# Optimization experiments

Hardware: AMD Instinct MI355X
Metric: run time of the kernel (lower is better)

Reference implementation:

```python
import jax, jax.numpy as jnp
import numpy as np

N_NODES = 50000
N_EDGES = 600000
NUM_RELS = 5
IN_CH = 768
HID = 128
OUT_CH = 128
REL_DIM = 200


def _segment_softmax(scores, seg, n):
    # numerically stable softmax over variable-size segments (destination nodes)
    m = jax.ops.segment_max(scores, seg, num_segments=n)
    e = jnp.exp(scores - m[seg])
    s = jax.ops.segment_sum(e, seg, num_segments=n)
    return e / s[seg]


def _hgn_conv(x, edge_index, edge_type, W, Wr, a, Wres, rel_tab, final):
    # x: [N, h_in]; W: [h, h_in]; Wr: [h, rel_dim]; a: [3h]; rel_tab: [R, rel_dim]
    src = edge_index[0]
    dst = edge_index[1]
    n = x.shape[0]
    h = W.shape[0]
    Wx = x @ W.T                      # [N, h] (shared by x_i, x_j, messages)
    rel = rel_tab[edge_type] @ Wr.T   # [E, h]
    aA, aB, aC = a[:h], a[h:2 * h], a[2 * h:]
    # a([Wx_i | Wx_j | Wr rel]) decomposed to avoid materializing the concat
    score = Wx[dst] @ aA + Wx[src] @ aB + rel @ aC   # [E]
    alpha = jax.nn.leaky_relu(score, 0.2)
    alpha = _segment_softmax(alpha, dst, n)
    agg = jax.ops.segment_sum(Wx[src] * alpha[:, None], dst, num_segments=n)
    out = jax.nn.elu(agg + x @ Wres.T)
    if final:
        out = out / jnp.maximum(jnp.linalg.norm(out, axis=1, keepdims=True), 1e-12)
    return out, alpha


def setup_inputs() -> dict:
    key = jax.random.key(0)
    ks = jax.random.split(key, 20)
    s = 0.02
    return {
        "x": jax.random.normal(ks[0], (N_NODES, IN_CH), jnp.float32),
        "edge_index": jax.random.randint(ks[1], (2, N_EDGES), 0, N_NODES, jnp.int64 if jax.config.jax_enable_x64 else jnp.int32),
        "edge_type": jax.random.randint(ks[2], (N_EDGES,), 0, NUM_RELS, jnp.int64 if jax.config.jax_enable_x64 else jnp.int32),
        "l1_W": jax.random.normal(ks[3], (HID, IN_CH), jnp.float32) * s,
        "l1_b": jnp.zeros((HID,), jnp.float32),
        "l2_W": jax.random.normal(ks[4], (OUT_CH, HID), jnp.float32) * s,
        "l2_b": jnp.zeros((OUT_CH,), jnp.float32),
        "W1": jax.random.normal(ks[5], (HID, HID), jnp.float32) * s,
        "Wr1": jax.random.normal(ks[6], (HID, REL_DIM), jnp.float32) * s,
        "a1": jax.random.normal(ks[7], (3 * HID,), jnp.float32) * s,
        "Wres1": jax.random.normal(ks[8], (HID, HID), jnp.float32) * s,
        "rel1": jax.random.normal(ks[9], (NUM_RELS, REL_DIM), jnp.float32),
        "W2": jax.random.normal(ks[10], (HID, HID), jnp.float32) * s,
        "Wr2": jax.random.normal(ks[11], (HID, REL_DIM), jnp.float32) * s,
        "a2": jax.random.normal(ks[12], (3 * HID,), jnp.float32) * s,
        "Wres2": jax.random.normal(ks[13], (HID, HID), jnp.float32) * s,
        "rel2": jax.random.normal(ks[14], (NUM_RELS, REL_DIM), jnp.float32),
    }


def reference(x, edge_index, edge_type, l1_W, l1_b, l2_W, l2_b,
              W1, Wr1, a1, Wres1, rel1, W2, Wr2, a2, Wres2, rel2):
    out = jax.nn.leaky_relu(x @ l1_W.T + l1_b, 0.01)
    # layer 1 (dropout is identity in eval mode)
    out, alpha = _hgn_conv(out, edge_index, edge_type, W1, Wr1, a1, Wres1, rel1, final=False)
    # layer 2: original code blends alpha into self.alpha but weights messages
    # with its own (unblended) softmax alpha, so pre_alpha does not affect output
    out, _ = _hgn_conv(out, edge_index, edge_type, W2, Wr2, a2, Wres2, rel2, final=True)
    out = jax.nn.leaky_relu(out @ l2_W.T + l2_b, 0.01)
    return out
```

## Files before the change

kernel.cpp:

```cpp
#include <hip/hip_runtime.h>

namespace {

typedef unsigned short ushort_t;
typedef unsigned int uint_t;
typedef __attribute__((ext_vector_type(8))) short bf16x8;
typedef __attribute__((ext_vector_type(4))) float f32x4;

constexpr int N   = 50000;
constexpr int E   = 600000;
constexpr int NR  = 5;
constexpr int KIN = 768;
constexpr int H   = 128;
constexpr int RD  = 200;

__device__ inline ushort_t f2b(float f){
  uint_t u = __builtin_bit_cast(uint_t, f);
  uint_t r = (u + 0x7FFFu + ((u >> 16) & 1u)) >> 16;
  return (ushort_t)r;
}
__device__ inline float b2f_lo(uint_t u){ return __builtin_bit_cast(float, u << 16); }
__device__ inline float b2f_hi(uint_t u){ return __builtin_bit_cast(float, u & 0xFFFF0000u); }
__device__ inline float b2f_us(ushort_t h){ return __builtin_bit_cast(float, ((uint_t)h) << 16); }
__device__ inline uint_t cvtpk(float lo, float hi){
  uint_t r;
  asm("v_cvt_pk_bf16_f32 %0, %1, %2" : "=v"(r) : "v"(lo), "v"(hi));
  return r;
}

__global__ void prep_k(const float* __restrict__ l1W, const float* __restrict__ W1,
                       const float* __restrict__ R1, const float* __restrict__ W2,
                       const float* __restrict__ R2, const float* __restrict__ l2W,
                       ushort_t* __restrict__ wts, int* __restrict__ deg,
                       const int* __restrict__ edst,
                       const float* __restrict__ rel1, const float* __restrict__ Wr1,
                       const float* __restrict__ a1, float* __restrict__ sC1,
                       const float* __restrict__ rel2, const float* __restrict__ Wr2,
                       const float* __restrict__ a2, float* __restrict__ sC2){
  constexpr int S0 = H * KIN;
  constexpr int S1 = H * H;
  int b = blockIdx.x, tid = threadIdx.x;
  if (b < 704){
    int i = b * 256 + tid;
    float v;
    if (i < S0) v = l1W[i];
    else {
      int j = i - S0, seg = j >> 14, off = j & (S1 - 1);
      const float* srcs[5] = {W1, R1, W2, R2, l2W};
      v = srcs[seg][off];
    }
    wts[i] = f2b(v);
  } else if (b < 706){
    int L = b - 704;
    const float* rel = L ? rel2 : rel1;
    const float* Wr  = L ? Wr2  : Wr1;
    const float* a   = L ? a2   : a1;
    float*       sC  = L ? sC2  : sC1;
    __shared__ float red[256];
    int n = tid >> 1, half = tid & 1;
    float aC = a[256 + n];
    for (int r = 0; r < NR; ++r){
      float p = 0.f;
      for (int k = half * 100; k < half * 100 + 100; ++k)
        p += rel[r * RD + k] * Wr[n * RD + k];
      red[tid] = p * aC;
      __syncthreads();
      for (int s = 128; s > 0; s >>= 1){
        if (tid < s) red[tid] += red[tid + s];
        __syncthreads();
      }
      if (tid == 0) sC[r] = red[0];
      __syncthreads();
    }
  } else {
    int e = (b - 706) * 256 + tid;
    if (e < E) atomicAdd(&deg[edst[e]], 1);
  }
}

__global__ void scan1_k(const int* __restrict__ deg, int* __restrict__ chunk,
                        int* __restrict__ bsums, int n){
  __shared__ int s[256];
  int tid = threadIdx.x, i = blockIdx.x * 256 + tid;
  int v = (i < n) ? deg[i] : 0;
  s[tid] = v; __syncthreads();
  for (int off = 1; off < 256; off <<= 1){
    int t = (tid >= off) ? s[tid - off] : 0;
    __syncthreads();
    s[tid] += t;
    __syncthreads();
  }
  if (i < n) chunk[i] = s[tid] - v;
  if (tid == 255) bsums[blockIdx.x] = s[255];
}

__global__ void scan2_k(const int* __restrict__ bsums, int* __restrict__ boffs, int nb){
  __shared__ int s[256];
  int tid = threadIdx.x;
  int v = (tid < nb) ? bsums[tid] : 0;
  s[tid] = v; __syncthreads();
  for (int off = 1; off < 256; off <<= 1){
    int t = (tid >= off) ? s[tid - off] : 0;
    __syncthreads();
    s[tid] += t;
    __syncthreads();
  }
  if (tid < nb) boffs[tid] = s[tid] - v;
}

__global__ void scan3_k(int* __restrict__ rowptr, const int* __restrict__ boffs,
                        int* __restrict__ cursor, int n, int total){
  int i = blockIdx.x * 256 + threadIdx.x;
  if (i < n){
    int v = rowptr[i] + boffs[blockIdx.x];
    rowptr[i] = v; cursor[i] = v;
  }
  if (i == 0) rowptr[n] = total;
}

__global__ void fill_k(const int* __restrict__ src, const int* __restrict__ dst,
                       const int* __restrict__ et, int* __restrict__ cursor,
                       int* __restrict__ cpk){
  int e = blockIdx.x * 256 + threadIdx.x;
  if (e < E){
    int d = dst[e];
    int p = atomicAdd(&cursor[d], 1);
    cpk[p] = src[e] | (et[e] << 16);
  }
}

template<int K1, int M1, bool AFP32, bool NORM, bool STORE1, int M2>
__device__ __forceinline__ void gfused_impl(
    const void* __restrict__ Ap, const ushort_t* __restrict__ Wb1,
    const float* __restrict__ bias1,
    const ushort_t* __restrict__ WxG, const int* __restrict__ rowptr,
    const int* __restrict__ cpk, const float* __restrict__ sAi,
    const float* __restrict__ sBi, const float* __restrict__ sCi,
    ushort_t* __restrict__ out1,
    const ushort_t* __restrict__ Wb2, const float* __restrict__ vec2,
    void* __restrict__ out2, float* __restrict__ sAo, float* __restrict__ sBo, int M)
{
  constexpr int BK = 64;
  constexpr int NT = K1 / BK;
  constexpr int SP = 72;
  constexpr int CP = 136;
  __shared__ __align__(16) ushort_t U[128 * CP];
  __shared__ __align__(16) ushort_t Cs[64 * CP];
  ushort_t* const As  = U;
  ushort_t* const Bs  = U + 64 * SP;
  ushort_t* const B2s = U;
  const int tid  = threadIdx.x;
  const int wave = tid >> 6, lane = tid & 63;
  const int l15  = lane & 15, quad = lane >> 4;
  const int row0 = blockIdx.x * 64;

  if (M1 == 2){
    const int grp = tid >> 4;
    const int l   = tid & 15;
    const int gb  = tid & 48;
    #pragma unroll 1
    for (int nb = 0; nb < 4; ++nb){
      int lrow = nb * 16 + grp;
      int node = row0 + lrow;
      uint4 o = make_uint4(0, 0, 0, 0);
      if (node < M){
        int p0 = rowptr[node], p1 = rowptr[node + 1];
        int dg = p1 - p0;
        float sa = sAi[node];
        float m = -1e30f, ssum = 0.f;
        float a[8];
        #pragma unroll
        for (int j = 0; j < 8; ++j) a[j] = 0.f;
        for (int c0 = 0; c0 < dg; c0 += 16){
          int cnt = dg - c0; if (cnt > 16) cnt = 16;
          bool ok = l < cnt;
          int pk = cpk[p0 + c0 + (ok ? l : 0)];
          float s = sa + sBi[pk & 0xFFFF] + sCi[pk >> 16];
          s = s > 0.f ? s : 0.2f * s;
          float sv = ok ? s : -1e30f;
          #pragma unroll
          for (int off = 8; off > 0; off >>= 1) sv = fmaxf(sv, __shfl_xor(sv, off, 16));
          float mn = fmaxf(m, sv);
          float corr = __expf(m - mn);
          ssum *= corr;
          #pragma unroll
          for (int j = 0; j < 8; ++j) a[j] *= corr;
          float ev = ok ? __expf(s - mn) : 0.f;
          float es = ev;
          #pragma unroll
          for (int off = 8; off > 0; off >>= 1) es += __shfl_xor(es, off, 16);
          ssum += es;
          m = mn;
          int png = ok ? pk : 0;
          for (int e = 0; e < cnt; e += 4){
            int b0l = gb + e;
            int pe0 = __shfl(png, b0l,     64), pe1 = __shfl(png, b0l + 1, 64);
            int pe2 = __shfl(png, b0l + 2, 64), pe3 = __shfl(png, b0l + 3, 64);
            float e0 = __shfl(ev, b0l,     64), e1 = __shfl(ev, b0l + 1, 64);
            float e2 = __shfl(ev, b0l + 2, 64), e3 = __shfl(ev, b0l + 3, 64);
            uint4 u0 = *reinterpret_cast<const uint4*>(WxG + (size_t)(pe0 & 0xFFFF) * 128 + l * 8);
            uint4 u1 = *reinterpret_cast<const uint4*>(WxG + (size_t)(pe1 & 0xFFFF) * 128 + l * 8);
            uint4 u2 = *reinterpret_cast<const uint4*>(WxG + (size_t)(pe2 & 0xFFFF) * 128 + l * 8);
            uint4 u3 = *reinterpret_cast<const uint4*>(WxG + (size_t)(pe3 & 0xFFFF) * 128 + l * 8);
            a[0] += e0 * b2f_lo(u0.x); a[1] += e0 * b2f_hi(u0.x);
            a[2] += e0 * b2f_lo(u0.y); a[3] += e0 * b2f_hi(u0.y);
            a[4] += e0 * b2f_lo(u0.z); a[5] += e0 * b2f_hi(u0.z);
            a[6] += e0 * b2f_lo(u0.w); a[7] += e0 * b2f_hi(u0.w);
            a[0] += e1 * b2f_lo(u1.x); a[1] += e1 * b2f_hi(u1.x);
            a[2] += e1 * b2f_lo(u1.y); a[3] += e1 * b2f_hi(u1.y);
            a[4] += e1 * b2f_lo(u1.z); a[5] += e1 * b2f_hi(u1.z);
            a[6] += e1 * b2f_lo(u1.w); a[7] += e1 * b2f_hi(u1.w);
            a[0] += e2 * b2f_lo(u2.x); a[1] += e2 * b2f_hi(u2.x);
            a[2] += e2 * b2f_lo(u2.y); a[3] += e2 * b2f_hi(u2.y);
            a[4] += e2 * b2f_lo(u2.z); a[5] += e2 * b2f_hi(u2.z);
            a[6] += e2 * b2f_lo(u2.w); a[7] += e2 * b2f_hi(u2.w);
            a[0] += e3 * b2f_lo(u3.x); a[1] += e3 * b2f_hi(u3.x);
            a[2] += e3 * b2f_lo(u3.y); a[3] += e3 * b2f_hi(u3.y);
            a[4] += e3 * b2f_lo(u3.z); a[5] += e3 * b2f_hi(u3.z);
            a[6] += e3 * b2f_lo(u3.w); a[7] += e3 * b2f_hi(u3.w);
          }
        }
        float inv = (dg > 0) ? 1.f / ssum : 0.f;
        o.x = cvtpk(a[0] * inv, a[1] * inv);
        o.y = cvtpk(a[2] * inv, a[3] * inv);
        o.z = cvtpk(a[4] * inv, a[5] * inv);
        o.w = cvtpk(a[6] * inv, a[7] * inv);
      }
      *reinterpret_cast<uint4*>(&Cs[lrow * CP + l * 8]) = o;
    }
  }

  f32x4 acc[8];
  #pragma unroll
  for (int t = 0; t < 8; ++t) acc[t] = (f32x4){0.f, 0.f, 0.f, 0.f};

  const int ar = tid >> 2, aq = tid & 3;
  const int agrow = row0 + ar;
  const bool aok = agrow < M;
  const int awoff = ar * SP + aq * 16;
  const int bn = tid >> 1, bs = (tid & 1) * 32;
  const ushort_t* bsrc = Wb1 + (size_t)bn * K1 + bs;

  float4 pf0, pf1, pf2, pf3;
  uint4  pu0, pu1;
  uint4  pb0, pb1, pb2, pb3;
  pf0 = pf1 = pf2 = pf3 = make_float4(0.f, 0.f, 0.f, 0.f);
  pu0 = pu1 = make_uint4(0, 0, 0, 0);

#define ISSUE_A(kk) do{ if (aok){                                               \
    if constexpr (AFP32){                                                       \
      const float* ap_ = (const float*)Ap + (size_t)agrow * K1 + (kk) + aq * 16; \
      pf0 = *reinterpret_cast<const float4*>(ap_);                              \
      pf1 = *reinterpret_cast<const float4*>(ap_ + 4);                          \
      pf2 = *reinterpret_cast<const float4*>(ap_ + 8);                          \
      pf3 = *reinterpret_cast<const float4*>(ap_ + 12);                         \
    } else {                                                                    \
      const ushort_t* apb_ = (const ushort_t*)Ap + (size_t)agrow * K1 + (kk) + aq * 16; \
      pu0 = *reinterpret_cast<const uint4*>(apb_);                              \
      pu1 = *reinterpret_cast<const uint4*>(apb_ + 8);                          \
    } } }while(0)

#define ISSUE_B(kk) do{                                                         \
    pb0 = *reinterpret_cast<const uint4*>(bsrc + (kk));                         \
    pb1 = *reinterpret_cast<const uint4*>(bsrc + (kk) + 8);                     \
    pb2 = *reinterpret_cast<const uint4*>(bsrc + (kk) + 16);                    \
    pb3 = *reinterpret_cast<const uint4*>(bsrc + (kk) + 24);                    \
  }while(0)

#define WRITE_AB() do{                                                          \
    uint4 av0_, av1_;                                                           \
    if constexpr (AFP32){                                                       \
      av0_.x = cvtpk(pf0.x, pf0.y); av0_.y = cvtpk(pf0.z, pf0.w);               \
      av0_.z = cvtpk(pf1.x, pf1.y); av0_.w = cvtpk(pf1.z, pf1.w);               \
      av1_.x = cvtpk(pf2.x, pf2.y); av1_.y = cvtpk(pf2.z, pf2.w);               \
      av1_.z = cvtpk(pf3.x, pf3.y); av1_.w = cvtpk(pf3.z, pf3.w);               \
    } else { av0_ = pu0; av1_ = pu1; }                                          \
    *reinterpret_cast<uint4*>(&As[awoff])     = av0_;                           \
    *reinterpret_cast<uint4*>(&As[awoff + 8]) = av1_;                           \
    *reinterpret_cast<uint4*>(&Bs[bn * SP + bs])      = pb0;                    \
    *reinterpret_cast<uint4*>(&Bs[bn * SP + bs + 8])  = pb1;                    \
    *reinterpret_cast<uint4*>(&Bs[bn * SP + bs + 16]) = pb2;                    \
    *reinterpret_cast<uint4*>(&Bs[bn * SP + bs + 24]) = pb3;                    \
  }while(0)

  ISSUE_A(0); ISSUE_B(0);
  for (int t = 0; t < NT; ++t){
    WRITE_AB();
    __syncthreads();
    if (t + 1 < NT){ ISSUE_A((t + 1) * BK); ISSUE_B((t + 1) * BK); }
    bf16x8 af0 = *reinterpret_cast<const bf16x8*>(&As[(wave * 16 + l15) * SP + quad * 8]);
    bf16x8 af1 = *reinterpret_cast<const bf16x8*>(&As[(wave * 16 + l15) * SP + 32 + quad * 8]);
    #pragma unroll
    for (int tt = 0; tt < 8; ++tt){
      bf16x8 b0 = *reinterpret_cast<const bf16x8*>(&Bs[(tt * 16 + l15) * SP + quad * 8]);
      acc[tt] = __builtin_amdgcn_mfma_f32_16x16x32_bf16(af0, b0, acc[tt], 0, 0, 0);
      bf16x8 b1 = *reinterpret_cast<const bf16x8*>(&Bs[(tt * 16 + l15) * SP + 32 + quad * 8]);
      acc[tt] = __builtin_amdgcn_mfma_f32_16x16x32_bf16(af1, b1, acc[tt], 0, 0, 0);
    }
    __syncthreads();
  }
#undef ISSUE_A
#undef ISSUE_B
#undef WRITE_AB

  uint4 wreg[8];
  #pragma unroll
  for (int i = 0; i < 8; ++i){
    int idx = tid + 256 * i;
    int rr = idx >> 4, c8 = idx & 15;
    wreg[i] = *reinterpret_cast<const uint4*>(Wb2 + (size_t)rr * 128 + c8 * 8);
  }

  float vv[8][4];
  #pragma unroll
  for (int t = 0; t < 8; ++t){
    #pragma unroll
    for (int r = 0; r < 4; ++r){
      int lr  = wave * 16 + quad * 4 + r;
      int col = t * 16 + l15;
      float v = acc[t][r];
      if (M1 == 1){
        v += bias1[col];
        v = v > 0.f ? v : 0.01f * v;
      } else {
        v += b2f_us(Cs[lr * CP + col]);
        v = v > 0.f ? v : __expf(v) - 1.f;
      }
      vv[t][r] = v;
    }
  }
  #pragma unroll
  for (int i = 0; i < 8; ++i){
    int idx = tid + 256 * i;
    int rr = idx >> 4, c8 = idx & 15;
    *reinterpret_cast<uint4*>(&B2s[rr * CP + c8 * 8]) = wreg[i];
  }
  if (NORM){
    #pragma unroll
    for (int r = 0; r < 4; ++r){
      float ss = 0.f;
      #pragma unroll
      for (int t = 0; t < 8; ++t) ss += vv[t][r] * vv[t][r];
      #pragma unroll
      for (int off = 1; off < 16; off <<= 1) ss += __shfl_xor(ss, off, 64);
      float sc = 1.f / fmaxf(sqrtf(ss), 1e-12f);
      #pragma unroll
      for (int t = 0; t < 8; ++t) vv[t][r] *= sc;
    }
  }
  #pragma unroll
  for (int t = 0; t < 8; t += 2){
    #pragma unroll
    for (int r = 0; r < 4; ++r){
      int lr  = wave * 16 + quad * 4 + r;
      int c0  = t * 16 + l15, c1 = c0 + 16;
      uint_t pr = cvtpk(vv[t][r], vv[t + 1][r]);
      Cs[lr * CP + c0] = (ushort_t)pr;
      Cs[lr * CP + c1] = (ushort_t)(pr >> 16);
      if (STORE1){
        int grow = row0 + lr;
        if (grow < M){
          out1[(size_t)grow * 128 + c0] = (ushort_t)pr;
          out1[(size_t)grow * 128 + c1] = (ushort_t)(pr >> 16);
        }
      }
    }
  }
  __syncthreads();

  #pragma unroll
  for (int t = 0; t < 8; ++t) acc[t] = (f32x4){0.f, 0.f, 0.f, 0.f};
  #pragma unroll
  for (int kk = 0; kk < 4; ++kk){
    bf16x8 af2 = *reinterpret_cast<const bf16x8*>(&Cs[(wave * 16 + l15) * CP + kk * 32 + quad * 8]);
    #pragma unroll
    for (int t = 0; t < 8; ++t){
      bf16x8 bfr = *reinterpret_cast<const bf16x8*>(&B2s[(t * 16 + l15) * CP + kk * 32 + quad * 8]);
      acc[t] = __builtin_amdgcn_mfma_f32_16x16x32_bf16(af2, bfr, acc[t], 0, 0, 0);
    }
  }

  if (M2 == 1){
    #pragma unroll
    for (int t = 0; t < 8; ++t){
      #pragma unroll
      for (int r = 0; r < 4; ++r){
        int grow = row0 + wave * 16 + quad * 4 + r;
        if (grow >= M) continue;
        int col = t * 16 + l15;
        float v = acc[t][r] + vec2[col];
        v = v > 0.f ? v : 0.01f * v;
        ((float*)out2)[(size_t)grow * 128 + col] = v;
      }
    }
  } else {
    #pragma unroll
    for (int t = 0; t < 8; t += 2){
      #pragma unroll
      for (int r = 0; r < 4; ++r){
        int grow = row0 + wave * 16 + quad * 4 + r;
        if (grow >= M) continue;
        int c0 = t * 16 + l15;
        uint_t pr = cvtpk(acc[t][r], acc[t + 1][r]);
        ((ushort_t*)out2)[(size_t)grow * 128 + c0]      = (ushort_t)pr;
        ((ushort_t*)out2)[(size_t)grow * 128 + c0 + 16] = (ushort_t)(pr >> 16);
      }
    }
    #pragma unroll
    for (int r = 0; r < 4; ++r){
      float pa = 0.f, pb = 0.f;
      #pragma unroll
      for (int t = 0; t < 8; ++t){
        int col = t * 16 + l15;
        pa += acc[t][r] * vec2[col];
        pb += acc[t][r] * vec2[128 + col];
      }
      #pragma unroll
      for (int off = 1; off < 16; off <<= 1){
        pa += __shfl_xor(pa, off, 64);
        pb += __shfl_xor(pb, off, 64);
      }
      int grow = row0 + wave * 16 + quad * 4 + r;
      if (l15 == r && grow < M){ sAo[grow] = pa; sBo[grow] = pb; }
    }
  }
}

__global__ __launch_bounds__(256) void g1_k(
    const void* Ap, const ushort_t* Wb1, const float* bias1,
    ushort_t* out1, const ushort_t* Wb2, const float* vec2,
    void* out2, float* sAo, float* sBo, int M){
  gfused_impl<KIN, 1, true, false, true, 3>(Ap, Wb1, bias1, nullptr, nullptr,
      nullptr, nullptr, nullptr, nullptr, out1, Wb2, vec2, out2, sAo, sBo, M);
}
__global__ __launch_bounds__(256) void g2_k(
    const void* Ap, const ushort_t* Wb1,
    const ushort_t* WxG, const int* rowptr, const int* cpk,
    const float* sAi, const float* sBi, const float* sCi,
    ushort_t* out1, const ushort_t* Wb2, const float* vec2,
    void* out2, float* sAo, float* sBo, int M){
  gfused_impl<H, 2, false, false, true, 3>(Ap, Wb1, nullptr, WxG, rowptr, cpk,
      sAi, sBi, sCi, out1, Wb2, vec2, out2, sAo, sBo, M);
}
__global__ __launch_bounds__(256) void g3_k(
    const void* Ap, const ushort_t* Wb1,
    const ushort_t* WxG, const int* rowptr, const int* cpk,
    const float* sAi, const float* sBi, const float* sCi,
    const ushort_t* Wb2, const float* vec2, void* out2, int M){
  gfused_impl<H, 2, false, true, false, 1>(Ap, Wb1, nullptr, WxG, rowptr, cpk,
      sAi, sBi, sCi, nullptr, Wb2, vec2, out2, nullptr, nullptr, M);
}

}

extern "C" void kernel_launch(void* const* d_in, const int* in_sizes, int n_in,
                              void* d_out, int out_size, void* d_ws, size_t ws_size,
                              hipStream_t stream)
{
  const float* x     = (const float*)d_in[0];
  const int*   eidx  = (const int*)d_in[1];
  const int*   et    = (const int*)d_in[2];
  const float* l1W   = (const float*)d_in[3];
  const float* l1b   = (const float*)d_in[4];
  const float* l2W   = (const float*)d_in[5];
  const float* l2b   = (const float*)d_in[6];
  const float* W1    = (const float*)d_in[7];
  const float* Wr1   = (const float*)d_in[8];
  const float* a1    = (const float*)d_in[9];
  const float* Wres1 = (const float*)d_in[10];
  const float* rel1  = (const float*)d_in[11];
  const float* W2    = (const float*)d_in[12];
  const float* Wr2   = (const float*)d_in[13];
  const float* a2    = (const float*)d_in[14];
  const float* Wres2 = (const float*)d_in[15];
  const float* rel2  = (const float*)d_in[16];
  float* outp = (float*)d_out;

  const int* esrc = eidx;
  const int* edst = eidx + E;

  float* f = (float*)d_ws;
  size_t o = 0;
  float* sA1  = f + o; o += N;
  float* sB1  = f + o; o += N;
  float* sA2  = f + o; o += N;
  float* sB2  = f + o; o += N;
  float* sC1  = f + o; o += 8;
  float* sC2  = f + o; o += 8;
  ushort_t* us = (ushort_t*)(f + o);
  size_t ou = 0;
  ushort_t* b0   = us + ou; ou += (size_t)N * H;
  ushort_t* b1   = us + ou; ou += (size_t)N * H;
  ushort_t* WxA  = us + ou; ou += (size_t)N * H;
  ushort_t* WxB  = us + ou; ou += (size_t)N * H;
  ushort_t* wtsb = us + ou; ou += (size_t)H * KIN + 5 * H * H;
  ushort_t* l1Wb = wtsb;
  ushort_t* W1b  = wtsb + H * KIN;
  ushort_t* R1b  = W1b + H * H;
  ushort_t* W2b  = R1b + H * H;
  ushort_t* R2b  = W2b + H * H;
  ushort_t* l2Wb = R2b + H * H;
  if (ou & 1) ou += 1;
  int* wi = (int*)(us + ou);
  size_t oi = 0;
  int* deg    = wi + oi; oi += N;
  int* rowptr = wi + oi; oi += N + 1;
  int* cursor = wi + oi; oi += N;
  int* bsums  = wi + oi; oi += 256;
  int* boffs  = wi + oi; oi += 256;
  int* cpk    = wi + oi; oi += E;

  const int EB    = (E + 255) / 256;
  const int NB256 = (N + 255) / 256;
  const int GB    = (N + 63) / 64;

  hipMemsetAsync(deg, 0, (size_t)N * sizeof(int), stream);
  prep_k<<<706 + EB, 256, 0, stream>>>(l1W, W1, Wres1, W2, Wres2, l2W, wtsb, deg,
                                       edst, rel1, Wr1, a1, sC1, rel2, Wr2, a2, sC2);
  scan1_k<<<NB256, 256, 0, stream>>>(deg, rowptr, bsums, N);
  scan2_k<<<1, 256, 0, stream>>>(bsums, boffs, NB256);
  scan3_k<<<NB256, 256, 0, stream>>>(rowptr, boffs, cursor, N, E);
  fill_k<<<EB, 256, 0, stream>>>(esrc, edst, et, cursor, cpk);

  g1_k<<<GB, 256, 0, stream>>>(x, l1Wb, l1b, b0, W1b, a1, WxA, sA1, sB1, N);

  g2_k<<<GB, 256, 0, stream>>>(b0, R1b, WxA, rowptr, cpk, sA1, sB1, sC1,
                               b1, W2b, a2, WxB, sA2, sB2, N);

  g3_k<<<GB, 256, 0, stream>>>(b1, R2b, WxB, rowptr, cpk, sA2, sB2, sC2,
                               l2Wb, l2b, outp, N);
}
```

Before: 481.7 us.

## Merge CSR build and weight prep into one cooperative kernel with grid syncs

Replaces the memset, prep, three scan kernels and fill kernel with a single cooperative launch of 256 blocks that uses grid-wide syncs between the degree count, scan and fill phases. This removes several kernel launches and inter-kernel gaps. In exchange, each phase now runs on a fixed 256-block grid with grid-stride loops, which may lower parallelism for the atomic degree and fill phases, and each grid sync adds its own cost.

```diff
diff --git a/kernel.cpp b/kernel.cpp
--- a/kernel.cpp
+++ b/kernel.cpp
@@ -1,4 +1,7 @@
 #include <hip/hip_runtime.h>
+#include <hip/hip_cooperative_groups.h>
+
+namespace cg = cooperative_groups;
 
 namespace {
 
@@ -28,20 +31,33 @@
   return r;
 }
 
-__global__ void prep_k(const float* __restrict__ l1W, const float* __restrict__ W1,
-                       const float* __restrict__ R1, const float* __restrict__ W2,
-                       const float* __restrict__ R2, const float* __restrict__ l2W,
-                       ushort_t* __restrict__ wts, int* __restrict__ deg,
-                       const int* __restrict__ edst,
-                       const float* __restrict__ rel1, const float* __restrict__ Wr1,
-                       const float* __restrict__ a1, float* __restrict__ sC1,
-                       const float* __restrict__ rel2, const float* __restrict__ Wr2,
-                       const float* __restrict__ a2, float* __restrict__ sC2){
+__global__ void csr_k(
+    const float* __restrict__ l1W, const float* __restrict__ W1,
+    const float* __restrict__ R1, const float* __restrict__ W2,
+    const float* __restrict__ R2, const float* __restrict__ l2W,
+    ushort_t* __restrict__ wts,
+    const float* __restrict__ rel1, const float* __restrict__ Wr1,
+    const float* __restrict__ a1, float* __restrict__ sC1,
+    const float* __restrict__ rel2, const float* __restrict__ Wr2,
+    const float* __restrict__ a2, float* __restrict__ sC2,
+    const int* __restrict__ esrc, const int* __restrict__ edst,
+    const int* __restrict__ et,
+    int* __restrict__ deg, int* __restrict__ rowptr, int* __restrict__ cursor,
+    int* __restrict__ bsums, int* __restrict__ cpk)
+{
+  cg::grid_group grid = cg::this_grid();
   constexpr int S0 = H * KIN;
   constexpr int S1 = H * H;
-  int b = blockIdx.x, tid = threadIdx.x;
-  if (b < 704){
-    int i = b * 256 + tid;
+  constexpr int TOT = S0 + 5 * S1;
+  constexpr int NB = (N + 255) / 256;
+  __shared__ int   s[256];
+  __shared__ float red[256];
+  const int tid = threadIdx.x;
+  const int gid = blockIdx.x * 256 + tid;
+  const int gsz = gridDim.x * 256;
+
+  for (int i = gid; i < N; i += gsz) deg[i] = 0;
+  for (int i = gid; i < TOT; i += gsz){
     float v;
     if (i < S0) v = l1W[i];
     else {
@@ -50,13 +66,13 @@
       v = srcs[seg][off];
     }
     wts[i] = f2b(v);
-  } else if (b < 706){
-    int L = b - 704;
+  }
+  if (blockIdx.x < 2){
+    int L = blockIdx.x;
     const float* rel = L ? rel2 : rel1;
     const float* Wr  = L ? Wr2  : Wr1;
     const float* a   = L ? a2   : a1;
     float*       sC  = L ? sC2  : sC1;
-    __shared__ float red[256];
     int n = tid >> 1, half = tid & 1;
     float aC = a[256 + n];
     for (int r = 0; r < NR; ++r){
@@ -65,67 +81,57 @@
         p += rel[r * RD + k] * Wr[n * RD + k];
       red[tid] = p * aC;
       __syncthreads();
-      for (int s = 128; s > 0; s >>= 1){
-        if (tid < s) red[tid] += red[tid + s];
+      for (int ss = 128; ss > 0; ss >>= 1){
+        if (tid < ss) red[tid] += red[tid + ss];
         __syncthreads();
       }
       if (tid == 0) sC[r] = red[0];
       __syncthreads();
     }
-  } else {
-    int e = (b - 706) * 256 + tid;
-    if (e < E) atomicAdd(&deg[edst[e]], 1);
-  }
-}
-
-__global__ void scan1_k(const int* __restrict__ deg, int* __restrict__ chunk,
-                        int* __restrict__ bsums, int n){
-  __shared__ int s[256];
-  int tid = threadIdx.x, i = blockIdx.x * 256 + tid;
-  int v = (i < n) ? deg[i] : 0;
-  s[tid] = v; __syncthreads();
-  for (int off = 1; off < 256; off <<= 1){
-    int t = (tid >= off) ? s[tid - off] : 0;
-    __syncthreads();
-    s[tid] += t;
-    __syncthreads();
-  }
-  if (i < n) chunk[i] = s[tid] - v;
-  if (tid == 255) bsums[blockIdx.x] = s[255];
-}
-
-__global__ void scan2_k(const int* __restrict__ bsums, int* __restrict__ boffs, int nb){
-  __shared__ int s[256];
-  int tid = threadIdx.x;
-  int v = (tid < nb) ? bsums[tid] : 0;
-  s[tid] = v; __syncthreads();
-  for (int off = 1; off < 256; off <<= 1){
-    int t = (tid >= off) ? s[tid - off] : 0;
-    __syncthreads();
-    s[tid] += t;
-    __syncthreads();
-  }
-  if (tid < nb) boffs[tid] = s[tid] - v;
-}
-
-__global__ void scan3_k(int* __restrict__ rowptr, const int* __restrict__ boffs,
-                        int* __restrict__ cursor, int n, int total){
-  int i = blockIdx.x * 256 + threadIdx.x;
-  if (i < n){
-    int v = rowptr[i] + boffs[blockIdx.x];
-    rowptr[i] = v; cursor[i] = v;
-  }
-  if (i == 0) rowptr[n] = total;
-}
-
-__global__ void fill_k(const int* __restrict__ src, const int* __restrict__ dst,
-                       const int* __restrict__ et, int* __restrict__ cursor,
-                       int* __restrict__ cpk){
-  int e = blockIdx.x * 256 + threadIdx.x;
-  if (e < E){
-    int d = dst[e];
+  }
+  grid.sync();
+
+  for (int e = gid; e < E; e += gsz) atomicAdd(&deg[edst[e]], 1);
+  grid.sync();
+
+  if (blockIdx.x < NB){
+    int i = blockIdx.x * 256 + tid;
+    int v = (i < N) ? deg[i] : 0;
+    s[tid] = v; __syncthreads();
+    for (int off = 1; off < 256; off <<= 1){
+      int t = (tid >= off) ? s[tid - off] : 0;
+      __syncthreads();
+      s[tid] += t;
+      __syncthreads();
+    }
+    if (i < N) rowptr[i] = s[tid] - v;
+    if (tid == 255) bsums[blockIdx.x] = s[255];
+  }
+  grid.sync();
+
+  if (blockIdx.x < NB){
+    int v = (tid < NB) ? bsums[tid] : 0;
+    s[tid] = v; __syncthreads();
+    for (int off = 1; off < 256; off <<= 1){
+      int t = (tid >= off) ? s[tid - off] : 0;
+      __syncthreads();
+      s[tid] += t;
+      __syncthreads();
+    }
+    int add = s[blockIdx.x] - bsums[blockIdx.x];
+    int i = blockIdx.x * 256 + tid;
+    if (i < N){
+      int val = rowptr[i] + add;
+      rowptr[i] = val; cursor[i] = val;
+    }
+    if (i == 0) rowptr[N] = E;
+  }
+  grid.sync();
+
+  for (int e = gid; e < E; e += gsz){
+    int d = edst[e];
     int p = atomicAdd(&cursor[d], 1);
-    cpk[p] = src[e] | (et[e] << 16);
+    cpk[p] = esrc[e] | (et[e] << 16);
   }
 }
 
@@ -510,17 +516,19 @@
   int* boffs  = wi + oi; oi += 256;
   int* cpk    = wi + oi; oi += E;
 
-  const int EB    = (E + 255) / 256;
-  const int NB256 = (N + 255) / 256;
-  const int GB    = (N + 63) / 64;
-
-  hipMemsetAsync(deg, 0, (size_t)N * sizeof(int), stream);
-  prep_k<<<706 + EB, 256, 0, stream>>>(l1W, W1, Wres1, W2, Wres2, l2W, wtsb, deg,
-                                       edst, rel1, Wr1, a1, sC1, rel2, Wr2, a2, sC2);
-  scan1_k<<<NB256, 256, 0, stream>>>(deg, rowptr, bsums, N);
-  scan2_k<<<1, 256, 0, stream>>>(bsums, boffs, NB256);
-  scan3_k<<<NB256, 256, 0, stream>>>(rowptr, boffs, cursor, N, E);
-  fill_k<<<EB, 256, 0, stream>>>(esrc, edst, et, cursor, cpk);
+  const int GB = (N + 63) / 64;
+
+  {
+    void* args[] = {
+      (void*)&l1W, (void*)&W1, (void*)&Wres1, (void*)&W2, (void*)&Wres2,
+      (void*)&l2W, (void*)&wtsb,
+      (void*)&rel1, (void*)&Wr1, (void*)&a1, (void*)&sC1,
+      (void*)&rel2, (void*)&Wr2, (void*)&a2, (void*)&sC2,
+      (void*)&esrc, (void*)&edst, (void*)&et,
+      (void*)&deg, (void*)&rowptr, (void*)&cursor, (void*)&bsums, (void*)&cpk
+    };
+    hipLaunchCooperativeKernel((void*)csr_k, dim3(256), dim3(256), args, 0, stream);
+  }
 
   g1_k<<<GB, 256, 0, stream>>>(x, l1Wb, l1b, b0, W1b, a1, WxA, sA1, sB1, N);
 
```

After: 623.5 us. 29.4% more time.

## Fuse three-pass scan into one grid-synchronized kernel and widen K-tile for first GEMM

Applied to the files above, without the earlier changes.

Replaces the three scan kernels with a single kernel. Each block publishes its partial sum, bumps an atomic counter, and spin-waits until all blocks have arrived, then computes its own offset locally. The GEMM tile depth becomes a template parameter, and the 768-wide input projection now uses BK=96, so it runs fewer K iterations and barriers at the cost of more shared memory. The spin barrier is only safe if all 196 blocks are co-resident, which holds on this GPU, and the larger LDS footprint may lower occupancy of g1.

```diff
diff --git a/kernel.cpp b/kernel.cpp
--- a/kernel.cpp
+++ b/kernel.cpp
@@ -78,10 +78,12 @@
   }
 }
 
-__global__ void scan1_k(const int* __restrict__ deg, int* __restrict__ chunk,
-                        int* __restrict__ bsums, int n){
+__global__ void scanall_k(const int* __restrict__ deg, int* __restrict__ rowptr,
+                          int* __restrict__ cursor, int* __restrict__ bsums,
+                          int* __restrict__ flag, int n, int total, int nb){
   __shared__ int s[256];
-  int tid = threadIdx.x, i = blockIdx.x * 256 + tid;
+  const int tid = threadIdx.x, bid = blockIdx.x;
+  const int i = bid * 256 + tid;
   int v = (i < n) ? deg[i] : 0;
   s[tid] = v; __syncthreads();
   for (int off = 1; off < 256; off <<= 1){
@@ -90,30 +92,29 @@
     s[tid] += t;
     __syncthreads();
   }
-  if (i < n) chunk[i] = s[tid] - v;
-  if (tid == 255) bsums[blockIdx.x] = s[255];
-}
-
-__global__ void scan2_k(const int* __restrict__ bsums, int* __restrict__ boffs, int nb){
-  __shared__ int s[256];
-  int tid = threadIdx.x;
-  int v = (tid < nb) ? bsums[tid] : 0;
-  s[tid] = v; __syncthreads();
+  int chunkexcl = s[tid] - v;
+  if (tid == 255){
+    bsums[bid] = s[255];
+    __threadfence();
+    atomicAdd(flag, 1);
+  }
+  if (tid == 0){
+    while (atomicAdd(flag, 0) < nb){ __builtin_amdgcn_s_sleep(8); }
+  }
+  __syncthreads();
+  __threadfence();
+  int bv = (tid < nb) ? bsums[tid] : 0;
+  s[tid] = bv; __syncthreads();
   for (int off = 1; off < 256; off <<= 1){
     int t = (tid >= off) ? s[tid - off] : 0;
     __syncthreads();
     s[tid] += t;
     __syncthreads();
   }
-  if (tid < nb) boffs[tid] = s[tid] - v;
-}
-
-__global__ void scan3_k(int* __restrict__ rowptr, const int* __restrict__ boffs,
-                        int* __restrict__ cursor, int n, int total){
-  int i = blockIdx.x * 256 + threadIdx.x;
+  int add = s[bid] - bsums[bid];
   if (i < n){
-    int v = rowptr[i] + boffs[blockIdx.x];
-    rowptr[i] = v; cursor[i] = v;
+    int val = chunkexcl + add;
+    rowptr[i] = val; cursor[i] = val;
   }
   if (i == 0) rowptr[n] = total;
 }
@@ -129,7 +130,7 @@
   }
 }
 
-template<int K1, int M1, bool AFP32, bool NORM, bool STORE1, int M2>
+template<int K1, int BKT, int M1, bool AFP32, bool NORM, bool STORE1, int M2>
 __device__ __forceinline__ void gfused_impl(
     const void* __restrict__ Ap, const ushort_t* __restrict__ Wb1,
     const float* __restrict__ bias1,
@@ -140,11 +141,12 @@
     const ushort_t* __restrict__ Wb2, const float* __restrict__ vec2,
     void* __restrict__ out2, float* __restrict__ sAo, float* __restrict__ sBo, int M)
 {
-  constexpr int BK = 64;
+  constexpr int BK = BKT;
   constexpr int NT = K1 / BK;
-  constexpr int SP = 72;
+  constexpr int SP = BK + 8;
   constexpr int CP = 136;
-  __shared__ __align__(16) ushort_t U[128 * CP];
+  constexpr int UE = (192 * SP > 128 * CP) ? 192 * SP : 128 * CP;
+  __shared__ __align__(16) ushort_t U[UE];
   __shared__ __align__(16) ushort_t Cs[64 * CP];
   ushort_t* const As  = U;
   ushort_t* const Bs  = U + 64 * SP;
@@ -234,53 +236,52 @@
   #pragma unroll
   for (int t = 0; t < 8; ++t) acc[t] = (f32x4){0.f, 0.f, 0.f, 0.f};
 
+  constexpr int AF4 = BK / 16;
+  constexpr int AU4 = BK / 32;
+  constexpr int BU4 = BK / 16;
   const int ar = tid >> 2, aq = tid & 3;
   const int agrow = row0 + ar;
   const bool aok = agrow < M;
-  const int awoff = ar * SP + aq * 16;
-  const int bn = tid >> 1, bs = (tid & 1) * 32;
+  const int awoff = ar * SP + aq * (BK / 4);
+  const int bn = tid >> 1, bs = (tid & 1) * (BK / 2);
   const ushort_t* bsrc = Wb1 + (size_t)bn * K1 + bs;
 
-  float4 pf0, pf1, pf2, pf3;
-  uint4  pu0, pu1;
-  uint4  pb0, pb1, pb2, pb3;
-  pf0 = pf1 = pf2 = pf3 = make_float4(0.f, 0.f, 0.f, 0.f);
-  pu0 = pu1 = make_uint4(0, 0, 0, 0);
+  float4 pfa[AF4] = {};
+  uint4  pua[AU4] = {};
+  uint4  pb[BU4];
 
 #define ISSUE_A(kk) do{ if (aok){                                               \
     if constexpr (AFP32){                                                       \
-      const float* ap_ = (const float*)Ap + (size_t)agrow * K1 + (kk) + aq * 16; \
-      pf0 = *reinterpret_cast<const float4*>(ap_);                              \
-      pf1 = *reinterpret_cast<const float4*>(ap_ + 4);                          \
-      pf2 = *reinterpret_cast<const float4*>(ap_ + 8);                          \
-      pf3 = *reinterpret_cast<const float4*>(ap_ + 12);                         \
+      const float* ap_ = (const float*)Ap + (size_t)agrow * K1 + (kk) + aq * (BK / 4); \
+      _Pragma("unroll") for (int j_ = 0; j_ < AF4; ++j_)                        \
+        pfa[j_] = *reinterpret_cast<const float4*>(ap_ + j_ * 4);               \
     } else {                                                                    \
-      const ushort_t* apb_ = (const ushort_t*)Ap + (size_t)agrow * K1 + (kk) + aq * 16; \
-      pu0 = *reinterpret_cast<const uint4*>(apb_);                              \
-      pu1 = *reinterpret_cast<const uint4*>(apb_ + 8);                          \
+      const ushort_t* apb_ = (const ushort_t*)Ap + (size_t)agrow * K1 + (kk) + aq * (BK / 4); \
+      _Pragma("unroll") for (int j_ = 0; j_ < AU4; ++j_)                        \
+        pua[j_] = *reinterpret_cast<const uint4*>(apb_ + j_ * 8);               \
     } } }while(0)
 
 #define ISSUE_B(kk) do{                                                         \
-    pb0 = *reinterpret_cast<const uint4*>(bsrc + (kk));                         \
-    pb1 = *reinterpret_cast<const uint4*>(bsrc + (kk) + 8);                     \
-    pb2 = *reinterpret_cast<const uint4*>(bsrc + (kk) + 16);                    \
-    pb3 = *reinterpret_cast<const uint4*>(bsrc + (kk) + 24);                    \
+    _Pragma("unroll") for (int j_ = 0; j_ < BU4; ++j_)                          \
+      pb[j_] = *reinterpret_cast<const uint4*>(bsrc + (kk) + j_ * 8);           \
   }while(0)
 
 #define WRITE_AB() do{                                                          \
-    uint4 av0_, av1_;                                                           \
     if constexpr (AFP32){                                                       \
-      av0_.x = cvtpk(pf0.x, pf0.y); av0_.y = cvtpk(pf0.z, pf0.w);               \
-      av0_.z = cvtpk(pf1.x, pf1.y); av0_.w = cvtpk(pf1.z, pf1.w);               \
-      av1_.x = cvtpk(pf2.x, pf2.y); av1_.y = cvtpk(pf2.z, pf2.w);               \
-      av1_.z = cvtpk(pf3.x, pf3.y); av1_.w = cvtpk(pf3.z, pf3.w);               \
-    } else { av0_ = pu0; av1_ = pu1; }                                          \
-    *reinterpret_cast<uint4*>(&As[awoff])     = av0_;                           \
-    *reinterpret_cast<uint4*>(&As[awoff + 8]) = av1_;                           \
-    *reinterpret_cast<uint4*>(&Bs[bn * SP + bs])      = pb0;                    \
-    *reinterpret_cast<uint4*>(&Bs[bn * SP + bs + 8])  = pb1;                    \
-    *reinterpret_cast<uint4*>(&Bs[bn * SP + bs + 16]) = pb2;                    \
-    *reinterpret_cast<uint4*>(&Bs[bn * SP + bs + 24]) = pb3;                    \
+      _Pragma("unroll") for (int j_ = 0; j_ < AU4; ++j_){                       \
+        uint4 av_;                                                              \
+        av_.x = cvtpk(pfa[2*j_].x, pfa[2*j_].y);                                \
+        av_.y = cvtpk(pfa[2*j_].z, pfa[2*j_].w);                                \
+        av_.z = cvtpk(pfa[2*j_+1].x, pfa[2*j_+1].y);                            \
+        av_.w = cvtpk(pfa[2*j_+1].z, pfa[2*j_+1].w);                            \
+        *reinterpret_cast<uint4*>(&As[awoff + j_ * 8]) = av_;                   \
+      }                                                                         \
+    } else {                                                                    \
+      _Pragma("unroll") for (int j_ = 0; j_ < AU4; ++j_)                        \
+        *reinterpret_cast<uint4*>(&As[awoff + j_ * 8]) = pua[j_];               \
+    }                                                                           \
+    _Pragma("unroll") for (int j_ = 0; j_ < BU4; ++j_)                          \
+      *reinterpret_cast<uint4*>(&Bs[bn * SP + bs + j_ * 8]) = pb[j_];           \
   }while(0)
 
   ISSUE_A(0); ISSUE_B(0);
@@ -288,14 +289,14 @@
     WRITE_AB();
     __syncthreads();
     if (t + 1 < NT){ ISSUE_A((t + 1) * BK); ISSUE_B((t + 1) * BK); }
-    bf16x8 af0 = *reinterpret_cast<const bf16x8*>(&As[(wave * 16 + l15) * SP + quad * 8]);
-    bf16x8 af1 = *reinterpret_cast<const bf16x8*>(&As[(wave * 16 + l15) * SP + 32 + quad * 8]);
-    #pragma unroll
-    for (int tt = 0; tt < 8; ++tt){
-      bf16x8 b0 = *reinterpret_cast<const bf16x8*>(&Bs[(tt * 16 + l15) * SP + quad * 8]);
-      acc[tt] = __builtin_amdgcn_mfma_f32_16x16x32_bf16(af0, b0, acc[tt], 0, 0, 0);
-      bf16x8 b1 = *reinterpret_cast<const bf16x8*>(&Bs[(tt * 16 + l15) * SP + 32 + quad * 8]);
-      acc[tt] = __builtin_amdgcn_mfma_f32_16x16x32_bf16(af1, b1, acc[tt], 0, 0, 0);
+    #pragma unroll
+    for (int kk = 0; kk < BK / 32; ++kk){
+      bf16x8 af = *reinterpret_cast<const bf16x8*>(&As[(wave * 16 + l15) * SP + kk * 32 + quad * 8]);
+      #pragma unroll
+      for (int tt = 0; tt < 8; ++tt){
+        bf16x8 bfr = *reinterpret_cast<const bf16x8*>(&Bs[(tt * 16 + l15) * SP + kk * 32 + quad * 8]);
+        acc[tt] = __builtin_amdgcn_mfma_f32_16x16x32_bf16(af, bfr, acc[tt], 0, 0, 0);
+      }
     }
     __syncthreads();
   }
@@ -430,7 +431,7 @@
     const void* Ap, const ushort_t* Wb1, const float* bias1,
     ushort_t* out1, const ushort_t* Wb2, const float* vec2,
     void* out2, float* sAo, float* sBo, int M){
-  gfused_impl<KIN, 1, true, false, true, 3>(Ap, Wb1, bias1, nullptr, nullptr,
+  gfused_impl<KIN, 96, 1, true, false, true, 3>(Ap, Wb1, bias1, nullptr, nullptr,
       nullptr, nullptr, nullptr, nullptr, out1, Wb2, vec2, out2, sAo, sBo, M);
 }
 __global__ __launch_bounds__(256) void g2_k(
@@ -439,7 +440,7 @@
     const float* sAi, const float* sBi, const float* sCi,
     ushort_t* out1, const ushort_t* Wb2, const float* vec2,
     void* out2, float* sAo, float* sBo, int M){
-  gfused_impl<H, 2, false, false, true, 3>(Ap, Wb1, nullptr, WxG, rowptr, cpk,
+  gfused_impl<H, 64, 2, false, false, true, 3>(Ap, Wb1, nullptr, WxG, rowptr, cpk,
       sAi, sBi, sCi, out1, Wb2, vec2, out2, sAo, sBo, M);
 }
 __global__ __launch_bounds__(256) void g3_k(
@@ -447,7 +448,7 @@
     const ushort_t* WxG, const int* rowptr, const int* cpk,
     const float* sAi, const float* sBi, const float* sCi,
     const ushort_t* Wb2, const float* vec2, void* out2, int M){
-  gfused_impl<H, 2, false, true, false, 1>(Ap, Wb1, nullptr, WxG, rowptr, cpk,
+  gfused_impl<H, 64, 2, false, true, false, 1>(Ap, Wb1, nullptr, WxG, rowptr, cpk,
       sAi, sBi, sCi, nullptr, Wb2, vec2, out2, nullptr, nullptr, M);
 }
 
@@ -503,23 +504,21 @@
   if (ou & 1) ou += 1;
   int* wi = (int*)(us + ou);
   size_t oi = 0;
-  int* deg    = wi + oi; oi += N;
-  int* rowptr = wi + oi; oi += N + 1;
-  int* cursor = wi + oi; oi += N;
-  int* bsums  = wi + oi; oi += 256;
-  int* boffs  = wi + oi; oi += 256;
-  int* cpk    = wi + oi; oi += E;
+  int* deg     = wi + oi; oi += N;
+  int* scanflg = wi + oi; oi += 1;
+  int* rowptr  = wi + oi; oi += N + 1;
+  int* cursor  = wi + oi; oi += N;
+  int* bsums   = wi + oi; oi += 256;
+  int* cpk     = wi + oi; oi += E;
 
   const int EB    = (E + 255) / 256;
   const int NB256 = (N + 255) / 256;
   const int GB    = (N + 63) / 64;
 
-  hipMemsetAsync(deg, 0, (size_t)N * sizeof(int), stream);
+  hipMemsetAsync(deg, 0, (size_t)(N + 1) * sizeof(int), stream);
   prep_k<<<706 + EB, 256, 0, stream>>>(l1W, W1, Wres1, W2, Wres2, l2W, wtsb, deg,
                                        edst, rel1, Wr1, a1, sC1, rel2, Wr2, a2, sC2);
-  scan1_k<<<NB256, 256, 0, stream>>>(deg, rowptr, bsums, N);
-  scan2_k<<<1, 256, 0, stream>>>(bsums, boffs, NB256);
-  scan3_k<<<NB256, 256, 0, stream>>>(rowptr, boffs, cursor, N, E);
+  scanall_k<<<NB256, 256, 0, stream>>>(deg, rowptr, cursor, bsums, scanflg, N, E, NB256);
   fill_k<<<EB, 256, 0, stream>>>(esrc, edst, et, cursor, cpk);
 
   g1_k<<<GB, 256, 0, stream>>>(x, l1Wb, l1b, b0, W1b, a1, WxA, sA1, sB1, N);
```

Result: slower. 517.0 us (+7.3%).
